# Performance work log

Hardware: AMD Instinct MI355X
Metric: run time of the kernel (lower is better)

Reference implementation:

```python
import jax, jax.numpy as jnp
import numpy as np

B, L, D, H = 1, 320, 128, 4
DH = D // H
LN_EPS = 1e-5


def setup_inputs() -> dict:
    key = jax.random.key(0)
    ks = jax.random.split(key, 4)
    z = jax.random.normal(ks[0], (B, L, L, D), jnp.float32)
    mask = jax.random.randint(ks[1], (B, L), 0, 2).astype(jnp.int32)
    ln_g = jnp.ones((D,), jnp.float32)
    ln_b = jnp.zeros((D,), jnp.float32)
    w_qkv = (jax.random.normal(ks[2], (3 * D, D), jnp.float32) * 0.02)
    b_qkv = jnp.zeros((3 * D,), jnp.float32)
    w_out = (jax.random.normal(ks[3], (D, D), jnp.float32) * 0.02)
    b_out = jnp.zeros((D,), jnp.float32)
    return {"z": z, "mask": mask, "ln_g": ln_g, "ln_b": ln_b,
            "w_qkv": w_qkv, "b_qkv": b_qkv, "w_out": w_out, "b_out": b_out}


def reference(z, mask, ln_g, ln_b, w_qkv, b_qkv, w_out, b_out):
    # z: (B, L, L, D), mask: (B, L) with 1 = keep, 0 = masked key
    mu = jnp.mean(z, axis=-1, keepdims=True)
    var = jnp.mean(jnp.square(z - mu), axis=-1, keepdims=True)
    zn = (z - mu) * jax.lax.rsqrt(var + LN_EPS) * ln_g + ln_b

    zf = zn.reshape(B * L, L, D)                       # row-wise: each of B*L rows is a length-L sequence
    qkv = zf @ w_qkv.T + b_qkv                         # (B*L, L, 3D)
    q, k, v = jnp.split(qkv, 3, axis=-1)

    def split_heads(x):
        return x.reshape(B * L, L, H, DH).transpose(0, 2, 1, 3)  # (B*L, H, L, DH)

    q, k, v = split_heads(q), split_heads(k), split_heads(v)
    scores = jnp.einsum('nhqd,nhkd->nhqk', q, k) / np.sqrt(DH).astype(np.float32)

    # additive -inf at masked key positions, shared across all L rows of a batch
    bias = jnp.where(mask > 0, 0.0, -jnp.inf).astype(scores.dtype)   # (B, L)
    bias = jnp.repeat(bias, L, axis=0)[:, None, None, :]             # (B*L, 1, 1, L)

    attn = jax.nn.softmax(scores + bias, axis=-1)
    o = jnp.einsum('nhqk,nhkd->nhqd', attn, v)
    o = o.transpose(0, 2, 1, 3).reshape(B * L, L, D)
    out = o @ w_out.T + b_out
    return z + out.reshape(B, L, L, D)
```

## Files before the change

kernel.cpp:

```cpp
#include <hip/hip_runtime.h>

#define LQ 320
#define NSEQ 320
#define NROWS (NSEQ*LQ)
#define DDIM 128
#define NH 4
#define DHD 32
#define LN_EPS 1e-5f
#define QSC2 0.25508652025545527f

typedef __bf16 bf16x8 __attribute__((ext_vector_type(8)));
typedef __bf16 bf16x2 __attribute__((ext_vector_type(2)));
typedef float f32x4 __attribute__((ext_vector_type(4)));
typedef float f32x16 __attribute__((ext_vector_type(16)));
union FragU { unsigned int u[4]; bf16x8 v; };

__device__ int g_inv[LQ];
__device__ int g_cnt;
__device__ __align__(16) unsigned short g_wbf[512 * DDIM];

__device__ inline unsigned short f2bf(float f) {
    return __builtin_bit_cast(unsigned short, (__bf16)f);
}
__device__ inline unsigned int pack2(float a, float b) {
    bf16x2 t;
    t[0] = (__bf16)a;
    t[1] = (__bf16)b;
    return __builtin_bit_cast(unsigned int, t);
}
__device__ inline void pl32swap(unsigned int &a, unsigned int &b) {
    asm volatile("v_permlane32_swap_b32 %0, %1" : "+v"(a), "+v"(b));
}

__global__ __launch_bounds__(256) void k0_ln(
    const float* __restrict__ z, const float* __restrict__ ln_g, const float* __restrict__ ln_b,
    unsigned int* __restrict__ znws, const int* __restrict__ mask,
    const float* __restrict__ w_qkv, const float* __restrict__ w_out)
{
    const int tid = threadIdx.x;
    const int bx = blockIdx.x;
    const int rowbase = bx * 64;
    const int lane = tid & 63;
    const int wid = tid >> 6;

    if (bx == 0) {
        if (tid < 64) {
            int carry = 0;
            #pragma unroll 1
            for (int c = 0; c < 5; ++c) {
                const int i = c * 64 + tid;
                const int m = (mask[i] > 0) ? 1 : 0;
                int v = m;
                #pragma unroll
                for (int off = 1; off < 64; off <<= 1) {
                    const int o = __shfl_up(v, off, 64);
                    if (tid >= off) v += o;
                }
                v += carry;
                if (m) g_inv[v - 1] = i;
                carry = __shfl(v, 63, 64);
            }
            if (tid == 0) g_cnt = carry;
            for (int s = carry + tid; s < LQ; s += 64) g_inv[s] = 0;
        }
    } else if (bx <= 32) {
        const int cid = (bx - 1) * 256 + tid;
        const int l2  = cid & 63;
        const int nt  = (cid >> 6) & 7;
        const int kt  = (cid >> 9) & 3;
        const int s4  = cid >> 11;
        const int qn2 = l2 & 15, gd2 = l2 >> 4;
        const int row = s4 * 128 + nt * 16 + qn2;
        const float4* src4 = (s4 < 3) ? (const float4*)w_qkv : (const float4*)w_out;
        const int rloc = (s4 < 3) ? row : (row - 384);
        const int fi = rloc * 32 + kt * 8 + gd2 * 2;
        const float4 a = src4[fi];
        const float4 b = src4[fi + 1];
        uint4 val;
        val.x = pack2(a.x, a.y);
        val.y = pack2(a.z, a.w);
        val.z = pack2(b.x, b.y);
        val.w = pack2(b.z, b.w);
        ((uint4*)g_wbf)[cid] = val;
    }

    const float g0 = ln_g[2 * lane], g1 = ln_g[2 * lane + 1];
    const float bb0 = ln_b[2 * lane], bb1 = ln_b[2 * lane + 1];
    #pragma unroll 1
    for (int r = wid; r < 64; r += 4) {
        const int row = rowbase + r;
        const float2 v = *(const float2*)(z + (size_t)row * DDIM + 2 * lane);
        float s = v.x + v.y;
        float s2 = v.x * v.x + v.y * v.y;
        #pragma unroll
        for (int off = 32; off > 0; off >>= 1) {
            s  += __shfl_xor(s, off, 64);
            s2 += __shfl_xor(s2, off, 64);
        }
        const float mu = s * (1.0f / 128.0f);
        const float var = s2 * (1.0f / 128.0f) - mu * mu;
        const float rs = rsqrtf(var + LN_EPS);
        znws[(size_t)row * 64 + lane] =
            pack2((v.x - mu) * rs * g0 + bb0, (v.y - mu) * rs * g1 + bb1);
    }
}

__global__ __launch_bounds__(256, 4) void k1_qkv(
    const unsigned short* __restrict__ znws, const float* __restrict__ b_qkv,
    unsigned short* __restrict__ qws, unsigned short* __restrict__ kws,
    unsigned short* __restrict__ vws)
{
    __shared__ unsigned short ldsb[17408];
    const int tid = threadIdx.x;
    const int bx = blockIdx.x;
    const int sect = bx % 3;
    const int mbase = (bx / 3) * 128;
    const int lane = tid & 63;
    const int wid = tid >> 6;
    const int qn = lane & 15, gd = lane >> 4;

    const int cnt = __builtin_amdgcn_readfirstlane(g_cnt);
    const int PT32 = (cnt + 31) & ~31;
    const int CP8  = (cnt + 7) & ~7;
    const int stride = (sect == 0) ? LQ : ((sect == 1) ? PT32 : CP8);
    const int rows_total = NSEQ * stride;
    if (mbase >= rows_total) return;

    {
        const uint4* src = (const uint4*)g_wbf + sect * 2048;
        uint4* dst = (uint4*)ldsb;
        #pragma unroll
        for (int i = 0; i < 8; ++i) dst[tid + i * 256] = src[tid + i * 256];
    }

    const int n0 = mbase / stride;
    const int s0 = mbase - n0 * stride;

    int arow[2];
    #pragma unroll
    for (int rg = 0; rg < 2; ++rg) {
        const int off = wid * 32 + rg * 16 + qn;
        int n = n0, s = s0 + off;
        while (s >= stride) { s -= stride; ++n; }
        int grow = n * LQ + ((sect == 0) ? s : g_inv[s]);
        if (mbase + off >= rows_total) grow = 0;
        arow[rg] = grow;
    }

    FragU afAll[2][4];
    #pragma unroll
    for (int rg = 0; rg < 2; ++rg)
        #pragma unroll
        for (int kt = 0; kt < 4; ++kt)
            afAll[rg][kt].v = *(const bf16x8*)&znws[(size_t)arow[rg] * DDIM + kt * 32 + gd * 8];

    __syncthreads();

    const f32x4 zero4 = {0.f, 0.f, 0.f, 0.f};
    f32x4 acc[2][8];
    #pragma unroll
    for (int rg = 0; rg < 2; ++rg)
        #pragma unroll
        for (int nt = 0; nt < 8; ++nt) acc[rg][nt] = zero4;

    #pragma unroll
    for (int kt = 0; kt < 4; ++kt) {
        #pragma unroll
        for (int nt = 0; nt < 8; ++nt) {
            FragU bf;
            bf.v = *(const bf16x8*)&ldsb[((kt * 8 + nt) * 64 + lane) * 8];
            #pragma unroll
            for (int rg = 0; rg < 2; ++rg)
                acc[rg][nt] = __builtin_amdgcn_mfma_f32_16x16x32_bf16(afAll[rg][kt].v, bf.v, acc[rg][nt], 0, 0, 0);
        }
    }

    float bq[8];
    #pragma unroll
    for (int nt = 0; nt < 8; ++nt) bq[nt] = b_qkv[sect * 128 + nt * 16 + qn];
    const float sc = (sect == 0) ? QSC2 : 1.0f;

    __syncthreads();
    unsigned short* tr = ldsb;

    if (sect < 2) {
        #pragma unroll
        for (int rg = 0; rg < 2; ++rg) {
            #pragma unroll
            for (int r = 0; r < 4; ++r) {
                const int row = wid * 32 + rg * 16 + 4 * gd + r;
                #pragma unroll
                for (int nt = 0; nt < 8; ++nt) {
                    const int col = nt * 16 + qn;
                    tr[row * 132 + col] = f2bf((acc[rg][nt][r] + bq[nt]) * sc);
                }
            }
        }
    } else {
        #pragma unroll
        for (int rg = 0; rg < 2; ++rg) {
            const int row0 = wid * 32 + rg * 16 + 4 * gd;
            #pragma unroll
            for (int nt = 0; nt < 8; ++nt) {
                const int col = nt * 16 + qn;
                uint2 pv;
                pv.x = pack2(acc[rg][nt][0] + bq[nt], acc[rg][nt][1] + bq[nt]);
                pv.y = pack2(acc[rg][nt][2] + bq[nt], acc[rg][nt][3] + bq[nt]);
                *(uint2*)&tr[col * 132 + row0] = pv;
            }
        }
    }
    __syncthreads();

    if (sect < 2) {
        unsigned short* dst = (sect == 0) ? qws : kws;
        #pragma unroll 1
        for (int k16 = 0; k16 < 16; ++k16) {
            const int o2 = lane * 4 + k16 * 256;
            const int i_loc = o2 >> 5, d = o2 & 31;
            if (mbase + i_loc < rows_total) {
                int n = n0, s = s0 + i_loc;
                while (s >= stride) { s -= stride; ++n; }
                const ushort4 val = *(const ushort4*)&tr[i_loc * 132 + wid * 32 + d];
                *(ushort4*)&dst[((size_t)(n * NH + wid) * LQ + s) * DHD + d] = val;
            }
        }
    } else {
        #pragma unroll 1
        for (int k16 = 0; k16 < 16; ++k16) {
            const int o2 = lane * 4 + k16 * 256;
            const int d = o2 >> 7, i_loc = o2 & 127;
            if (mbase + i_loc < rows_total) {
                int n = n0, s = s0 + i_loc;
                while (s >= stride) { s -= stride; ++n; }
                const ushort4 val = *(const ushort4*)&tr[(wid * 32 + d) * 132 + i_loc];
                *(ushort4*)&vws[(size_t)(n * NH + wid) * (DHD * LQ) + d * CP8 + s] = val;
            }
        }
    }
}

__global__ __launch_bounds__(320, 4) void k2_attn_mfma(
    const unsigned short* __restrict__ qws, const unsigned short* __restrict__ kws,
    const unsigned short* __restrict__ vtws, unsigned short* __restrict__ ows)
{
    const int tid = threadIdx.x;
    const int bx = blockIdx.x;
    const int nh = bx >> 1;
    const int lane = tid & 63;
    const int wid = tid >> 6;
    const int qt = (bx & 1) * 5 + wid;
    const int qc = lane & 31;
    const int hf = lane >> 5;

    const int cnt = __builtin_amdgcn_readfirstlane(g_cnt);
    const int PT32 = (cnt + 31) & ~31;
    const int CP8  = (cnt + 7) & ~7;
    const int NT   = PT32 >> 5;

    const int n = nh >> 2, h = nh & 3;
    const unsigned short* kb = kws + (size_t)nh * LQ * DHD + hf * 8;
    const unsigned short* vb = vtws + (size_t)nh * DHD * LQ + (size_t)qc * CP8 + hf * 8;
    const unsigned short* qp = qws + ((size_t)nh * LQ + qt * 32 + qc) * DHD + hf * 8;

    FragU qf1, qf2;
    qf1.v = *(const bf16x8*)qp;
    qf2.v = *(const bf16x8*)(qp + 16);

    f32x16 o;
    #pragma unroll
    for (int r = 0; r < 16; ++r) o[r] = 0.f;
    float m_run = -1e30f, l_run = 0.f;

    FragU kf1, kf2, vf1, vf2;
    {
        const unsigned short* kr = kb + (size_t)qc * DHD;
        kf1.v = *(const bf16x8*)kr;
        kf2.v = *(const bf16x8*)(kr + 16);
        vf1.v = *(const bf16x8*)(vb);
        vf2.v = *(const bf16x8*)(vb + 16);
    }

    #pragma unroll 1
    for (int kt = 0; kt < NT; ++kt) {
        FragU kf1n, kf2n, vf1n, vf2n;
        if (kt + 1 < NT) {
            const unsigned short* krn = kb + (size_t)((kt + 1) * 32 + qc) * DHD;
            kf1n.v = *(const bf16x8*)krn;
            kf2n.v = *(const bf16x8*)(krn + 16);
            vf1n.v = *(const bf16x8*)(vb + (kt + 1) * 32);
            vf2n.v = *(const bf16x8*)(vb + (kt + 1) * 32 + 16);
        }

        f32x16 c0;
        #pragma unroll
        for (int r = 0; r < 16; ++r) c0[r] = 0.f;
        if ((kt + 1) * 32 > cnt) {
            #pragma unroll
            for (int r = 0; r < 16; ++r) {
                const int krow = kt * 32 + (r & 3) + 8 * (r >> 2) + 4 * hf;
                c0[r] = (krow < cnt) ? 0.f : -1e30f;
            }
        }
        f32x16 st = __builtin_amdgcn_mfma_f32_32x32x16_bf16(kf1.v, qf1.v, c0, 0, 0, 0);
        st = __builtin_amdgcn_mfma_f32_32x32x16_bf16(kf2.v, qf2.v, st, 0, 0, 0);

        float mh = st[0];
        #pragma unroll
        for (int r = 1; r < 16; ++r) mh = fmaxf(mh, st[r]);
        mh = fmaxf(mh, __shfl_xor(mh, 32, 64));
        if (!__all(mh <= m_run + 8.0f)) {
            const float m_new = fmaxf(m_run, mh);
            const float scl = __builtin_amdgcn_exp2f(m_run - m_new);
            l_run *= scl;
            #pragma unroll
            for (int r = 0; r < 16; ++r) o[r] *= scl;
            m_run = m_new;
        }
        #pragma unroll
        for (int r = 0; r < 16; ++r) st[r] = __builtin_amdgcn_exp2f(st[r] - m_run);
        l_run += (((st[0] + st[1]) + (st[2] + st[3])) + ((st[4] + st[5]) + (st[6] + st[7])))
               + (((st[8] + st[9]) + (st[10] + st[11])) + ((st[12] + st[13]) + (st[14] + st[15])));

        unsigned int a01 = pack2(st[0], st[1]), a23 = pack2(st[2], st[3]);
        unsigned int a45 = pack2(st[4], st[5]), a67 = pack2(st[6], st[7]);
        pl32swap(a01, a45);
        pl32swap(a23, a67);
        FragU pa1;
        pa1.u[0] = a01; pa1.u[1] = a23; pa1.u[2] = a45; pa1.u[3] = a67;
        o = __builtin_amdgcn_mfma_f32_32x32x16_bf16(pa1.v, vf1.v, o, 0, 0, 0);

        unsigned int b01 = pack2(st[8], st[9]),  b23 = pack2(st[10], st[11]);
        unsigned int b45 = pack2(st[12], st[13]), b67 = pack2(st[14], st[15]);
        pl32swap(b01, b45);
        pl32swap(b23, b67);
        FragU pa2;
        pa2.u[0] = b01; pa2.u[1] = b23; pa2.u[2] = b45; pa2.u[3] = b67;
        o = __builtin_amdgcn_mfma_f32_32x32x16_bf16(pa2.v, vf2.v, o, 0, 0, 0);

        kf1 = kf1n; kf2 = kf2n; vf1 = vf1n; vf2 = vf2n;
    }

    l_run += __shfl_xor(l_run, 32, 64);
    const float inv = 1.0f / l_run;

    #pragma unroll
    for (int r = 0; r < 16; ++r) {
        const int qloc = (r & 3) + 8 * (r >> 2) + 4 * hf;
        const float iv = __shfl(inv, qloc, 64);
        const int qg = qt * 32 + qloc;
        ows[((size_t)(n * LQ + qg)) * DDIM + h * DHD + qc] = f2bf(o[r] * iv);
    }
}

__global__ __launch_bounds__(256, 4) void k3_out(
    const unsigned short* __restrict__ ows,
    const float* __restrict__ b_out, const float* __restrict__ z,
    float* __restrict__ out)
{
    __shared__ unsigned short ldsb[16384];
    const int tid = threadIdx.x;
    const int mbase = blockIdx.x * 128;
    const int lane = tid & 63;
    const int wid = tid >> 6;
    const int qn = lane & 15, gd = lane >> 4;

    {
        const uint4* src = (const uint4*)g_wbf + 3 * 2048;
        uint4* dst = (uint4*)ldsb;
        #pragma unroll
        for (int i = 0; i < 8; ++i) dst[tid + i * 256] = src[tid + i * 256];
    }

    FragU afAll[2][4];
    #pragma unroll
    for (int rg = 0; rg < 2; ++rg)
        #pragma unroll
        for (int kt = 0; kt < 4; ++kt)
            afAll[rg][kt].v = *(const bf16x8*)&ows[
                (size_t)(mbase + wid * 32 + rg * 16 + qn) * DDIM + kt * 32 + gd * 8];

    __syncthreads();

    const f32x4 zero4 = {0.f, 0.f, 0.f, 0.f};
    f32x4 acc[2][8];
    #pragma unroll
    for (int rg = 0; rg < 2; ++rg)
        #pragma unroll
        for (int nt = 0; nt < 8; ++nt) acc[rg][nt] = zero4;

    #pragma unroll
    for (int kt = 0; kt < 4; ++kt) {
        #pragma unroll
        for (int nt = 0; nt < 8; ++nt) {
            FragU bf;
            bf.v = *(const bf16x8*)&ldsb[((kt * 8 + nt) * 64 + lane) * 8];
            #pragma unroll
            for (int rg = 0; rg < 2; ++rg)
                acc[rg][nt] = __builtin_amdgcn_mfma_f32_16x16x32_bf16(afAll[rg][kt].v, bf.v, acc[rg][nt], 0, 0, 0);
        }
    }

    float bb[8];
    #pragma unroll
    for (int nt = 0; nt < 8; ++nt) bb[nt] = b_out[nt * 16 + qn];

    #pragma unroll
    for (int rg = 0; rg < 2; ++rg) {
        #pragma unroll
        for (int r = 0; r < 4; ++r) {
            const int grow = mbase + wid * 32 + rg * 16 + 4 * gd + r;
            const float* zr = z + (size_t)grow * DDIM;
            float* outr = out + (size_t)grow * DDIM;
            #pragma unroll
            for (int nt = 0; nt < 8; ++nt) {
                const int cg = nt * 16 + qn;
                outr[cg] = acc[rg][nt][r] + bb[nt] + zr[cg];
            }
        }
    }
}

extern "C" void kernel_launch(void* const* d_in, const int* in_sizes, int n_in,
                              void* d_out, int out_size, void* d_ws, size_t ws_size,
                              hipStream_t stream) {
    const float* z     = (const float*)d_in[0];
    const int*   mask  = (const int*)d_in[1];
    const float* ln_g  = (const float*)d_in[2];
    const float* ln_b  = (const float*)d_in[3];
    const float* w_qkv = (const float*)d_in[4];
    const float* b_qkv = (const float*)d_in[5];
    const float* w_out = (const float*)d_in[6];
    const float* b_out = (const float*)d_in[7];
    float* out = (float*)d_out;

    unsigned short* ws = (unsigned short*)d_ws;
    const size_t qE = (size_t)NSEQ * NH * LQ * DHD;
    unsigned short* qws = ws;
    unsigned short* kws = qws + qE;
    unsigned short* vws = kws + qE;
    unsigned short* shared_rgn = vws + qE;
    unsigned int*   znws = (unsigned int*)shared_rgn;
    unsigned short* ows  = shared_rgn;

    hipLaunchKernelGGL(k0_ln, dim3(NROWS / 64), dim3(256), 0, stream,
                       z, ln_g, ln_b, znws, mask, w_qkv, w_out);
    hipLaunchKernelGGL(k1_qkv, dim3(2400), dim3(256), 0, stream,
                       (const unsigned short*)znws, b_qkv, qws, kws, vws);
    hipLaunchKernelGGL(k2_attn_mfma, dim3(2560), dim3(320), 0, stream,
                       qws, kws, vws, ows);
    hipLaunchKernelGGL(k3_out, dim3(800), dim3(256), 0, stream,
                       ows, b_out, z, out);
}
```

Measured before the change: 198.0 us.

## Process two query tiles per wave in attention to reuse K/V fragments

Each wave in the attention kernel now handles two 32-row query tiles (wid and wid+5), so one block covers all ten query tiles of a sequence-head. Each K/V fragment load now feeds two sets of MFMAs, halving the global K/V reads and the grid size. The explicit next-iteration prefetch is removed and launch bounds drop to 3 blocks per CU to make room for the doubled accumulators. This raises register pressure and lowers occupancy, and more load latency may be exposed without the prefetch.

Measured after the change: 197.7 us. About the same (-0.1%).

```diff
diff --git a/kernel.cpp b/kernel.cpp
--- a/kernel.cpp
+++ b/kernel.cpp
@@ -240,16 +240,14 @@
     }
 }
 
-__global__ __launch_bounds__(320, 4) void k2_attn_mfma(
+__global__ __launch_bounds__(320, 3) void k2_attn_mfma(
     const unsigned short* __restrict__ qws, const unsigned short* __restrict__ kws,
     const unsigned short* __restrict__ vtws, unsigned short* __restrict__ ows)
 {
     const int tid = threadIdx.x;
-    const int bx = blockIdx.x;
-    const int nh = bx >> 1;
+    const int nh = blockIdx.x;
     const int lane = tid & 63;
     const int wid = tid >> 6;
-    const int qt = (bx & 1) * 5 + wid;
     const int qc = lane & 31;
     const int hf = lane >> 5;
 
@@ -261,36 +259,31 @@
     const int n = nh >> 2, h = nh & 3;
     const unsigned short* kb = kws + (size_t)nh * LQ * DHD + hf * 8;
     const unsigned short* vb = vtws + (size_t)nh * DHD * LQ + (size_t)qc * CP8 + hf * 8;
-    const unsigned short* qp = qws + ((size_t)nh * LQ + qt * 32 + qc) * DHD + hf * 8;
-
-    FragU qf1, qf2;
-    qf1.v = *(const bf16x8*)qp;
-    qf2.v = *(const bf16x8*)(qp + 16);
-
-    f32x16 o;
-    #pragma unroll
-    for (int r = 0; r < 16; ++r) o[r] = 0.f;
-    float m_run = -1e30f, l_run = 0.f;
-
-    FragU kf1, kf2, vf1, vf2;
-    {
-        const unsigned short* kr = kb + (size_t)qc * DHD;
+
+    const int qtA = wid, qtB = wid + 5;
+    const unsigned short* qpA = qws + ((size_t)nh * LQ + qtA * 32 + qc) * DHD + hf * 8;
+    const unsigned short* qpB = qws + ((size_t)nh * LQ + qtB * 32 + qc) * DHD + hf * 8;
+
+    FragU qfA1, qfA2, qfB1, qfB2;
+    qfA1.v = *(const bf16x8*)qpA;
+    qfA2.v = *(const bf16x8*)(qpA + 16);
+    qfB1.v = *(const bf16x8*)qpB;
+    qfB2.v = *(const bf16x8*)(qpB + 16);
+
+    f32x16 oA, oB;
+    #pragma unroll
+    for (int r = 0; r < 16; ++r) { oA[r] = 0.f; oB[r] = 0.f; }
+    float mA = -1e30f, lA = 0.f;
+    float mB = -1e30f, lB = 0.f;
+
+    #pragma unroll 1
+    for (int kt = 0; kt < NT; ++kt) {
+        const unsigned short* kr = kb + (size_t)(kt * 32 + qc) * DHD;
+        FragU kf1, kf2, vf1, vf2;
         kf1.v = *(const bf16x8*)kr;
         kf2.v = *(const bf16x8*)(kr + 16);
-        vf1.v = *(const bf16x8*)(vb);
-        vf2.v = *(const bf16x8*)(vb + 16);
-    }
-
-    #pragma unroll 1
-    for (int kt = 0; kt < NT; ++kt) {
-        FragU kf1n, kf2n, vf1n, vf2n;
-        if (kt + 1 < NT) {
-            const unsigned short* krn = kb + (size_t)((kt + 1) * 32 + qc) * DHD;
-            kf1n.v = *(const bf16x8*)krn;
-            kf2n.v = *(const bf16x8*)(krn + 16);
-            vf1n.v = *(const bf16x8*)(vb + (kt + 1) * 32);
-            vf2n.v = *(const bf16x8*)(vb + (kt + 1) * 32 + 16);
-        }
+        vf1.v = *(const bf16x8*)(vb + kt * 32);
+        vf2.v = *(const bf16x8*)(vb + kt * 32 + 16);
 
         f32x16 c0;
         #pragma unroll
@@ -302,54 +295,94 @@
                 c0[r] = (krow < cnt) ? 0.f : -1e30f;
             }
         }
-        f32x16 st = __builtin_amdgcn_mfma_f32_32x32x16_bf16(kf1.v, qf1.v, c0, 0, 0, 0);
-        st = __builtin_amdgcn_mfma_f32_32x32x16_bf16(kf2.v, qf2.v, st, 0, 0, 0);
-
-        float mh = st[0];
-        #pragma unroll
-        for (int r = 1; r < 16; ++r) mh = fmaxf(mh, st[r]);
-        mh = fmaxf(mh, __shfl_xor(mh, 32, 64));
-        if (!__all(mh <= m_run + 8.0f)) {
-            const float m_new = fmaxf(m_run, mh);
-            const float scl = __builtin_amdgcn_exp2f(m_run - m_new);
-            l_run *= scl;
-            #pragma unroll
-            for (int r = 0; r < 16; ++r) o[r] *= scl;
-            m_run = m_new;
-        }
-        #pragma unroll
-        for (int r = 0; r < 16; ++r) st[r] = __builtin_amdgcn_exp2f(st[r] - m_run);
-        l_run += (((st[0] + st[1]) + (st[2] + st[3])) + ((st[4] + st[5]) + (st[6] + st[7])))
-               + (((st[8] + st[9]) + (st[10] + st[11])) + ((st[12] + st[13]) + (st[14] + st[15])));
-
-        unsigned int a01 = pack2(st[0], st[1]), a23 = pack2(st[2], st[3]);
-        unsigned int a45 = pack2(st[4], st[5]), a67 = pack2(st[6], st[7]);
-        pl32swap(a01, a45);
-        pl32swap(a23, a67);
-        FragU pa1;
-        pa1.u[0] = a01; pa1.u[1] = a23; pa1.u[2] = a45; pa1.u[3] = a67;
-        o = __builtin_amdgcn_mfma_f32_32x32x16_bf16(pa1.v, vf1.v, o, 0, 0, 0);
-
-        unsigned int b01 = pack2(st[8], st[9]),  b23 = pack2(st[10], st[11]);
-        unsigned int b45 = pack2(st[12], st[13]), b67 = pack2(st[14], st[15]);
-        pl32swap(b01, b45);
-        pl32swap(b23, b67);
-        FragU pa2;
-        pa2.u[0] = b01; pa2.u[1] = b23; pa2.u[2] = b45; pa2.u[3] = b67;
-        o = __builtin_amdgcn_mfma_f32_32x32x16_bf16(pa2.v, vf2.v, o, 0, 0, 0);
-
-        kf1 = kf1n; kf2 = kf2n; vf1 = vf1n; vf2 = vf2n;
-    }
-
-    l_run += __shfl_xor(l_run, 32, 64);
-    const float inv = 1.0f / l_run;
+        f32x16 stA = __builtin_amdgcn_mfma_f32_32x32x16_bf16(kf1.v, qfA1.v, c0, 0, 0, 0);
+        f32x16 stB = __builtin_amdgcn_mfma_f32_32x32x16_bf16(kf1.v, qfB1.v, c0, 0, 0, 0);
+        stA = __builtin_amdgcn_mfma_f32_32x32x16_bf16(kf2.v, qfA2.v, stA, 0, 0, 0);
+        stB = __builtin_amdgcn_mfma_f32_32x32x16_bf16(kf2.v, qfB2.v, stB, 0, 0, 0);
+
+        {
+            float mh = stA[0];
+            #pragma unroll
+            for (int r = 1; r < 16; ++r) mh = fmaxf(mh, stA[r]);
+            mh = fmaxf(mh, __shfl_xor(mh, 32, 64));
+            if (!__all(mh <= mA + 8.0f)) {
+                const float m_new = fmaxf(mA, mh);
+                const float scl = __builtin_amdgcn_exp2f(mA - m_new);
+                lA *= scl;
+                #pragma unroll
+                for (int r = 0; r < 16; ++r) oA[r] *= scl;
+                mA = m_new;
+            }
+            #pragma unroll
+            for (int r = 0; r < 16; ++r) stA[r] = __builtin_amdgcn_exp2f(stA[r] - mA);
+            lA += (((stA[0] + stA[1]) + (stA[2] + stA[3])) + ((stA[4] + stA[5]) + (stA[6] + stA[7])))
+                + (((stA[8] + stA[9]) + (stA[10] + stA[11])) + ((stA[12] + stA[13]) + (stA[14] + stA[15])));
+
+            unsigned int a01 = pack2(stA[0], stA[1]), a23 = pack2(stA[2], stA[3]);
+            unsigned int a45 = pack2(stA[4], stA[5]), a67 = pack2(stA[6], stA[7]);
+            pl32swap(a01, a45);
+            pl32swap(a23, a67);
+            FragU pa1;
+            pa1.u[0] = a01; pa1.u[1] = a23; pa1.u[2] = a45; pa1.u[3] = a67;
+            oA = __builtin_amdgcn_mfma_f32_32x32x16_bf16(pa1.v, vf1.v, oA, 0, 0, 0);
+
+            unsigned int b01 = pack2(stA[8], stA[9]),  b23 = pack2(stA[10], stA[11]);
+            unsigned int b45 = pack2(stA[12], stA[13]), b67 = pack2(stA[14], stA[15]);
+            pl32swap(b01, b45);
+            pl32swap(b23, b67);
+            FragU pa2;
+            pa2.u[0] = b01; pa2.u[1] = b23; pa2.u[2] = b45; pa2.u[3] = b67;
+            oA = __builtin_amdgcn_mfma_f32_32x32x16_bf16(pa2.v, vf2.v, oA, 0, 0, 0);
+        }
+
+        {
+            float mh = stB[0];
+            #pragma unroll
+            for (int r = 1; r < 16; ++r) mh = fmaxf(mh, stB[r]);
+            mh = fmaxf(mh, __shfl_xor(mh, 32, 64));
+            if (!__all(mh <= mB + 8.0f)) {
+                const float m_new = fmaxf(mB, mh);
+                const float scl = __builtin_amdgcn_exp2f(mB - m_new);
+                lB *= scl;
+                #pragma unroll
+                for (int r = 0; r < 16; ++r) oB[r] *= scl;
+                mB = m_new;
+            }
+            #pragma unroll
+            for (int r = 0; r < 16; ++r) stB[r] = __builtin_amdgcn_exp2f(stB[r] - mB);
+            lB += (((stB[0] + stB[1]) + (stB[2] + stB[3])) + ((stB[4] + stB[5]) + (stB[6] + stB[7])))
+                + (((stB[8] + stB[9]) + (stB[10] + stB[11])) + ((stB[12] + stB[13]) + (stB[14] + stB[15])));
+
+            unsigned int a01 = pack2(stB[0], stB[1]), a23 = pack2(stB[2], stB[3]);
+            unsigned int a45 = pack2(stB[4], stB[5]), a67 = pack2(stB[6], stB[7]);
+            pl32swap(a01, a45);
+            pl32swap(a23, a67);
+            FragU pa1;
+            pa1.u[0] = a01; pa1.u[1] = a23; pa1.u[2] = a45; pa1.u[3] = a67;
+            oB = __builtin_amdgcn_mfma_f32_32x32x16_bf16(pa1.v, vf1.v, oB, 0, 0, 0);
+
+            unsigned int b01 = pack2(stB[8], stB[9]),  b23 = pack2(stB[10], stB[11]);
+            unsigned int b45 = pack2(stB[12], stB[13]), b67 = pack2(stB[14], stB[15]);
+            pl32swap(b01, b45);
+            pl32swap(b23, b67);
+            FragU pa2;
+            pa2.u[0] = b01; pa2.u[1] = b23; pa2.u[2] = b45; pa2.u[3] = b67;
+            oB = __builtin_amdgcn_mfma_f32_32x32x16_bf16(pa2.v, vf2.v, oB, 0, 0, 0);
+        }
+    }
+
+    lA += __shfl_xor(lA, 32, 64);
+    lB += __shfl_xor(lB, 32, 64);
+    const float invA = 1.0f / lA;
+    const float invB = 1.0f / lB;
 
     #pragma unroll
     for (int r = 0; r < 16; ++r) {
         const int qloc = (r & 3) + 8 * (r >> 2) + 4 * hf;
-        const float iv = __shfl(inv, qloc, 64);
-        const int qg = qt * 32 + qloc;
-        ows[((size_t)(n * LQ + qg)) * DDIM + h * DHD + qc] = f2bf(o[r] * iv);
+        const float ivA = __shfl(invA, qloc, 64);
+        const float ivB = __shfl(invB, qloc, 64);
+        ows[((size_t)(n * LQ + qtA * 32 + qloc)) * DDIM + h * DHD + qc] = f2bf(oA[r] * ivA);
+        ows[((size_t)(n * LQ + qtB * 32 + qloc)) * DDIM + h * DHD + qc] = f2bf(oB[r] * ivB);
     }
 }
 
@@ -447,7 +480,7 @@
                        z, ln_g, ln_b, znws, mask, w_qkv, w_out);
     hipLaunchKernelGGL(k1_qkv, dim3(2400), dim3(256), 0, stream,
                        (const unsigned short*)znws, b_qkv, qws, kws, vws);
-    hipLaunchKernelGGL(k2_attn_mfma, dim3(2560), dim3(320), 0, stream,
+    hipLaunchKernelGGL(k2_attn_mfma, dim3(1280), dim3(320), 0, stream,
                        qws, kws, vws, ows);
     hipLaunchKernelGGL(k3_out, dim3(800), dim3(256), 0, stream,
                        ows, b_out, z, out);
```
